# Kernel optimization log

Measured on AMD Instinct MI355X. Metric: run time of the kernel, lower is better.

The kernel has to match this reference:

```python
import jax, jax.numpy as jnp
import numpy as np

LN2 = 0.6931471805599453

def _logcosh(z):
    # numerically stable log(cosh(z)) = logaddexp(z, -z) - log(2)
    return jnp.logaddexp(z, -z) - LN2

def _logpsi(z, W, b, a):
    # RBM log-amplitude. z: [..., N] -> scalar per leading dims
    return z @ a + jnp.sum(_logcosh(z @ W + b), axis=-1)

def setup_inputs() -> dict:
    key = jax.random.key(0)
    k0, k1, k2, k3, k4 = jax.random.split(key, 5)
    B, N, H = 64, 512, 2048
    # spin configurations (sign pattern; flips y_k = x with site k negated work for any real values)
    x = jnp.sign(jax.random.normal(k0, (B, N), dtype=jnp.float32))
    # small init so exp(logpsi_y - logpsi_x) stays well-scaled
    W = 0.01 * jax.random.normal(k1, (N, H), dtype=jnp.float32)
    b = 0.01 * jax.random.normal(k2, (H,), dtype=jnp.float32)
    a = 0.01 * jax.random.normal(k3, (N,), dtype=jnp.float32)
    # per-connection operator matrix elements O(x, y_k)
    Oxy = jax.random.normal(k4, (N,), dtype=jnp.float32)
    return {"x": x, "W": W, "b": b, "a": a, "Oxy": Oxy}

def reference(x, W, b, a, Oxy):
    # eval_local_operator, vmapped over a batch of configurations.
    # operator.conn(x): y[k] = x with spin k flipped, with matrix element Oxy[k].
    B, N = x.shape
    flip = 1.0 - 2.0 * jnp.eye(N, dtype=x.dtype)          # [K=N, N]
    y = x[:, None, :] * flip[None, :, :]                  # [B, K, N] connected states
    logpsi_x = _logpsi(x, W, b, a)                        # [B]
    logpsi_y = _logpsi(y, W, b, a)                        # [B, K]
    # Oxy @ exp(logpsi_y - logpsi_x) per sample
    return jnp.einsum('k,bk->b', Oxy, jnp.exp(logpsi_y - logpsi_x[:, None]))
```

## Files before the change

### kernel.cpp

```cpp
#include <hip/hip_runtime.h>
#include <hip/hip_bf16.h>
#include <math.h>

constexpr int NB = 64;
constexpr int NN = 512;
constexpr int NH = 2048;
constexpr float LN2 = 0.6931471805599453f;

constexpr size_t OFF_TT = 0;

__global__ __launch_bounds__(512) void k_theta(const float* __restrict__ W,
                                               const float* __restrict__ x,
                                               const float* __restrict__ bvec,
                                               float* __restrict__ Tt,
                                               float* __restrict__ out) {
    __shared__ float sm[10240];
    int tid = threadIdx.x;
    int gb = blockIdx.x;
    int ht = gb & 31;
    int bt = gb >> 5;
    {
        int j = tid >> 5, c = tid & 31;
        const float4* xr = (const float4*)(x + (size_t)(bt * 16 + j) * NN);
#pragma unroll
        for (int i = 0; i < 4; i++) {
            float4 v = xr[c + i * 32];
            int n0 = (c + i * 32) * 4;
            sm[(n0 + 0) * 20 + j] = v.x;
            sm[(n0 + 1) * 20 + j] = v.y;
            sm[(n0 + 2) * 20 + j] = v.z;
            sm[(n0 + 3) * 20 + j] = v.w;
        }
    }
    __syncthreads();
    int hl = tid & 63, ns = tid >> 6;
    int h  = ht * 64 + hl;
    float acc[16];
#pragma unroll
    for (int j = 0; j < 16; j++) acc[j] = 0.f;
    const float* wp = W + h;
#pragma unroll 4
    for (int n = ns * 64; n < ns * 64 + 64; n++) {
        float w = wp[(size_t)n * NH];
        const float4* xv = (const float4*)(sm + n * 20);
        float4 a0 = xv[0], a1 = xv[1], a2 = xv[2], a3 = xv[3];
        acc[0]  = fmaf(a0.x, w, acc[0]);  acc[1]  = fmaf(a0.y, w, acc[1]);
        acc[2]  = fmaf(a0.z, w, acc[2]);  acc[3]  = fmaf(a0.w, w, acc[3]);
        acc[4]  = fmaf(a1.x, w, acc[4]);  acc[5]  = fmaf(a1.y, w, acc[5]);
        acc[6]  = fmaf(a1.z, w, acc[6]);  acc[7]  = fmaf(a1.w, w, acc[7]);
        acc[8]  = fmaf(a2.x, w, acc[8]);  acc[9]  = fmaf(a2.y, w, acc[9]);
        acc[10] = fmaf(a2.z, w, acc[10]); acc[11] = fmaf(a2.w, w, acc[11]);
        acc[12] = fmaf(a3.x, w, acc[12]); acc[13] = fmaf(a3.y, w, acc[13]);
        acc[14] = fmaf(a3.z, w, acc[14]); acc[15] = fmaf(a3.w, w, acc[15]);
    }
    __syncthreads();
    float4* r4 = (float4*)sm;
#pragma unroll
    for (int q = 0; q < 4; q++)
        r4[(ns * 1024 + hl * 16) / 4 + q] =
            make_float4(acc[q*4], acc[q*4+1], acc[q*4+2], acc[q*4+3]);
    __syncthreads();
#pragma unroll
    for (int o = tid; o < 1024; o += 512) {
        int hl2 = o >> 4, j2 = o & 15;
        float th = bvec[ht * 64 + hl2];
#pragma unroll
        for (int n2 = 0; n2 < 8; n2++) th += sm[n2 * 1024 + hl2 * 16 + j2];
        float ay = fabsf(th);
        float e  = __expf(-2.0f * ay);
        Tt[(size_t)(ht * 64 + hl2) * NB + bt * 16 + j2] =
            copysignf((1.0f - e) / (1.0f + e), th);
    }
    if (gb == 0 && tid < NB) out[tid] = 0.f;
}

__global__ __launch_bounds__(512) void k_main(const float* __restrict__ W,
                                              const float* __restrict__ Tt,
                                              const float* __restrict__ x,
                                              const float* __restrict__ a,
                                              const float* __restrict__ Oxy,
                                              float* __restrict__ out) {
    __shared__ float t2s[2 * NH];
    __shared__ float red[16 * NB];
    int tid = threadIdx.x;
    int lane = tid & 63, wv = tid >> 6;
    int k0 = __builtin_amdgcn_readfirstlane(blockIdx.x * 2);
    int hb = wv * 256;

    const float2* w0 = (const float2*)(W + (size_t)k0 * NH + hb);
    const float2* w1 = (const float2*)(W + (size_t)(k0 + 1) * NH + hb);
    float lc0 = 0.f, lc1 = 0.f;
#pragma unroll
    for (int i = 0; i < 2; i++) {
        float2 wa = w0[lane + i * 64];
        float2 wb = w1[lane + i * 64];
        float in[4] = {wa.x, wa.y, wb.x, wb.y};
        float t[4];
#pragma unroll
        for (int j = 0; j < 4; j++) {
            float y  = 2.0f * in[j];
            float ay = fabsf(y);
            float e  = __expf(-2.0f * ay);
            t[j] = copysignf((1.0f - e) / (1.0f + e), y);
            float l = ay + __logf(1.0f + e) - LN2;
            if (j < 2) lc0 += l; else lc1 += l;
        }
        int h2 = hb + (lane + i * 64) * 2;
        *(float4*)&t2s[h2 * 2] = make_float4(t[0], t[2], t[1], t[3]);
    }
#pragma unroll
    for (int off = 32; off > 0; off >>= 1) {
        lc0 += __shfl_xor(lc0, off);
        lc1 += __shfl_xor(lc1, off);
    }
    float ms0 = -x[(size_t)lane * NN + k0];
    float ms1 = -x[(size_t)lane * NN + k0 + 1];
    __syncthreads();

    float lp0 = lc0, lp1 = lc1;
    for (int h0 = hb; h0 < hb + 256; h0 += 32) {
        float p0 = 1.f, p1 = 1.f;
#pragma unroll
        for (int hh = 0; hh < 32; hh++) {
            int h = h0 + hh;
            float2 t = *(const float2*)&t2s[h * 2];
            float T = Tt[(size_t)h * NB + lane];
            p0 *= fmaf(t.x * T, ms0, 1.0f);
            p1 *= fmaf(t.y * T, ms1, 1.0f);
        }
        lp0 += __logf(p0);
        lp1 += __logf(p1);
    }
    red[(wv * 2 + 0) * NB + lane] = lp0;
    red[(wv * 2 + 1) * NB + lane] = lp1;
    __syncthreads();
    if (tid < NB) {
        float d0 = 2.0f * ms0 * a[k0];
        float d1 = 2.0f * ms1 * a[k0 + 1];
#pragma unroll
        for (int w2 = 0; w2 < 8; w2++) {
            d0 += red[(w2 * 2 + 0) * NB + tid];
            d1 += red[(w2 * 2 + 1) * NB + tid];
        }
        float c = Oxy[k0] * __expf(d0) + Oxy[k0 + 1] * __expf(d1);
        atomicAdd(&out[tid], c);
    }
}

extern "C" void kernel_launch(void* const* d_in, const int* in_sizes, int n_in,
                              void* d_out, int out_size, void* d_ws, size_t ws_size,
                              hipStream_t stream) {
    const float* x    = (const float*)d_in[0];
    const float* W    = (const float*)d_in[1];
    const float* bvec = (const float*)d_in[2];
    const float* a    = (const float*)d_in[3];
    const float* Oxy  = (const float*)d_in[4];
    float* out = (float*)d_out;

    float* Tt = (float*)d_ws + OFF_TT;

    k_theta<<<128, 512, 0, stream>>>(W, x, bvec, Tt, out);
    k_main<<<NN / 2, 512, 0, stream>>>(W, Tt, x, a, Oxy, out);
}
```

Before: 90.39 us.

## Fuse theta and main kernels into one cooperative kernel with grid sync

Merges the two kernel launches into a single cooperative launch of 256 blocks. Phase one computes the tanh(theta) table with 8-batch tiles over 256 blocks, then a grid-wide sync hands off to the per-flip product phase. The T table is also re-laid out in groups of four h values so the inner loop issues float4 loads, and the two per-site tanh vectors are split into separate shared arrays. This removes a launch gap and the separate kernel's tail at the cost of grid-sync overhead and a cooperative-launch requirement.

```diff
diff --git a/kernel.cpp b/kernel.cpp
--- a/kernel.cpp
+++ b/kernel.cpp
@@ -1,149 +1,151 @@
 #include <hip/hip_runtime.h>
-#include <hip/hip_bf16.h>
+#include <hip/hip_cooperative_groups.h>
 #include <math.h>
+
+namespace cg = cooperative_groups;
 
 constexpr int NB = 64;
 constexpr int NN = 512;
 constexpr int NH = 2048;
 constexpr float LN2 = 0.6931471805599453f;
 
-constexpr size_t OFF_TT = 0;
 
-__global__ __launch_bounds__(512) void k_theta(const float* __restrict__ W,
+__global__ __launch_bounds__(512) void k_fused(const float* __restrict__ W,
                                                const float* __restrict__ x,
                                                const float* __restrict__ bvec,
-                                               float* __restrict__ Tt,
+                                               const float* __restrict__ a,
+                                               const float* __restrict__ Oxy,
+                                               float* __restrict__ Tt4,
                                                float* __restrict__ out) {
-    __shared__ float sm[10240];
+    __shared__ float sm[6144];
     int tid = threadIdx.x;
-    int gb = blockIdx.x;
-    int ht = gb & 31;
-    int bt = gb >> 5;
+    int bid = blockIdx.x;
+
     {
-        int j = tid >> 5, c = tid & 31;
-        const float4* xr = (const float4*)(x + (size_t)(bt * 16 + j) * NN);
+        int ht  = bid & 31;
+        int btb = bid >> 5;
+        {
+            int j = tid >> 6, c = tid & 63;
+            const float4* xr = (const float4*)(x + (size_t)(btb * 8 + j) * NN);
 #pragma unroll
-        for (int i = 0; i < 4; i++) {
-            float4 v = xr[c + i * 32];
-            int n0 = (c + i * 32) * 4;
-            sm[(n0 + 0) * 20 + j] = v.x;
-            sm[(n0 + 1) * 20 + j] = v.y;
-            sm[(n0 + 2) * 20 + j] = v.z;
-            sm[(n0 + 3) * 20 + j] = v.w;
+            for (int i = 0; i < 2; i++) {
+                float4 v = xr[c + i * 64];
+                int n0 = (c + i * 64) * 4;
+                sm[(n0 + 0) * 12 + j] = v.x;
+                sm[(n0 + 1) * 12 + j] = v.y;
+                sm[(n0 + 2) * 12 + j] = v.z;
+                sm[(n0 + 3) * 12 + j] = v.w;
+            }
         }
-    }
-    __syncthreads();
-    int hl = tid & 63, ns = tid >> 6;
-    int h  = ht * 64 + hl;
-    float acc[16];
+        __syncthreads();
+        int hl = tid & 63, ns = tid >> 6;
+        float acc[8];
 #pragma unroll
-    for (int j = 0; j < 16; j++) acc[j] = 0.f;
-    const float* wp = W + h;
+        for (int q = 0; q < 8; q++) acc[q] = 0.f;
+        const float* wp = W + ht * 64 + hl;
 #pragma unroll 4
-    for (int n = ns * 64; n < ns * 64 + 64; n++) {
-        float w = wp[(size_t)n * NH];
-        const float4* xv = (const float4*)(sm + n * 20);
-        float4 a0 = xv[0], a1 = xv[1], a2 = xv[2], a3 = xv[3];
-        acc[0]  = fmaf(a0.x, w, acc[0]);  acc[1]  = fmaf(a0.y, w, acc[1]);
-        acc[2]  = fmaf(a0.z, w, acc[2]);  acc[3]  = fmaf(a0.w, w, acc[3]);
-        acc[4]  = fmaf(a1.x, w, acc[4]);  acc[5]  = fmaf(a1.y, w, acc[5]);
-        acc[6]  = fmaf(a1.z, w, acc[6]);  acc[7]  = fmaf(a1.w, w, acc[7]);
-        acc[8]  = fmaf(a2.x, w, acc[8]);  acc[9]  = fmaf(a2.y, w, acc[9]);
-        acc[10] = fmaf(a2.z, w, acc[10]); acc[11] = fmaf(a2.w, w, acc[11]);
-        acc[12] = fmaf(a3.x, w, acc[12]); acc[13] = fmaf(a3.y, w, acc[13]);
-        acc[14] = fmaf(a3.z, w, acc[14]); acc[15] = fmaf(a3.w, w, acc[15]);
-    }
-    __syncthreads();
-    float4* r4 = (float4*)sm;
-#pragma unroll
-    for (int q = 0; q < 4; q++)
-        r4[(ns * 1024 + hl * 16) / 4 + q] =
-            make_float4(acc[q*4], acc[q*4+1], acc[q*4+2], acc[q*4+3]);
-    __syncthreads();
-#pragma unroll
-    for (int o = tid; o < 1024; o += 512) {
-        int hl2 = o >> 4, j2 = o & 15;
+        for (int n = ns * 64; n < ns * 64 + 64; n++) {
+            float w = wp[(size_t)n * NH];
+            const float4* xv = (const float4*)(sm + n * 12);
+            float4 a0 = xv[0], a1 = xv[1];
+            acc[0] = fmaf(a0.x, w, acc[0]); acc[1] = fmaf(a0.y, w, acc[1]);
+            acc[2] = fmaf(a0.z, w, acc[2]); acc[3] = fmaf(a0.w, w, acc[3]);
+            acc[4] = fmaf(a1.x, w, acc[4]); acc[5] = fmaf(a1.y, w, acc[5]);
+            acc[6] = fmaf(a1.z, w, acc[6]); acc[7] = fmaf(a1.w, w, acc[7]);
+        }
+        __syncthreads();
+        float4* r4 = (float4*)sm;
+        r4[ns * 128 + hl * 2 + 0] = make_float4(acc[0], acc[1], acc[2], acc[3]);
+        r4[ns * 128 + hl * 2 + 1] = make_float4(acc[4], acc[5], acc[6], acc[7]);
+        __syncthreads();
+        int hl2 = tid >> 3, j2 = tid & 7;
         float th = bvec[ht * 64 + hl2];
 #pragma unroll
-        for (int n2 = 0; n2 < 8; n2++) th += sm[n2 * 1024 + hl2 * 16 + j2];
+        for (int n2 = 0; n2 < 8; n2++) th += sm[n2 * 512 + hl2 * 8 + j2];
         float ay = fabsf(th);
         float e  = __expf(-2.0f * ay);
-        Tt[(size_t)(ht * 64 + hl2) * NB + bt * 16 + j2] =
-            copysignf((1.0f - e) / (1.0f + e), th);
+        float T  = copysignf((1.0f - e) / (1.0f + e), th);
+        int h = ht * 64 + hl2, b = btb * 8 + j2;
+        Tt4[(size_t)(h >> 2) * 256 + b * 4 + (h & 3)] = T;
+        if (bid == 0 && tid < NB) out[tid] = 0.f;
     }
-    if (gb == 0 && tid < NB) out[tid] = 0.f;
-}
+    cg::this_grid().sync();
 
-__global__ __launch_bounds__(512) void k_main(const float* __restrict__ W,
-                                              const float* __restrict__ Tt,
-                                              const float* __restrict__ x,
-                                              const float* __restrict__ a,
-                                              const float* __restrict__ Oxy,
-                                              float* __restrict__ out) {
-    __shared__ float t2s[2 * NH];
-    __shared__ float red[16 * NB];
-    int tid = threadIdx.x;
-    int lane = tid & 63, wv = tid >> 6;
-    int k0 = __builtin_amdgcn_readfirstlane(blockIdx.x * 2);
-    int hb = wv * 256;
+    {
+        float* t2s0 = sm;
+        float* t2s1 = sm + NH;
+        float* red  = sm + 2 * NH;
+        int lane = tid & 63, wv = tid >> 6;
+        int k0 = __builtin_amdgcn_readfirstlane(blockIdx.x * 2);
+        int hb = wv * 256;
 
-    const float2* w0 = (const float2*)(W + (size_t)k0 * NH + hb);
-    const float2* w1 = (const float2*)(W + (size_t)(k0 + 1) * NH + hb);
-    float lc0 = 0.f, lc1 = 0.f;
+        const float2* w0 = (const float2*)(W + (size_t)k0 * NH + hb);
+        const float2* w1 = (const float2*)(W + (size_t)(k0 + 1) * NH + hb);
+        float lc0 = 0.f, lc1 = 0.f;
 #pragma unroll
-    for (int i = 0; i < 2; i++) {
-        float2 wa = w0[lane + i * 64];
-        float2 wb = w1[lane + i * 64];
-        float in[4] = {wa.x, wa.y, wb.x, wb.y};
-        float t[4];
+        for (int i = 0; i < 2; i++) {
+            float2 wa = w0[lane + i * 64];
+            float2 wb = w1[lane + i * 64];
+            float in[4] = {wa.x, wa.y, wb.x, wb.y};
+            float t[4];
 #pragma unroll
-        for (int j = 0; j < 4; j++) {
-            float y  = 2.0f * in[j];
-            float ay = fabsf(y);
-            float e  = __expf(-2.0f * ay);
-            t[j] = copysignf((1.0f - e) / (1.0f + e), y);
-            float l = ay + __logf(1.0f + e) - LN2;
-            if (j < 2) lc0 += l; else lc1 += l;
+            for (int q = 0; q < 4; q++) {
+                float y  = 2.0f * in[q];
+                float ay = fabsf(y);
+                float e  = __expf(-2.0f * ay);
+                t[q] = copysignf((1.0f - e) / (1.0f + e), y);
+                float l = ay + __logf(1.0f + e) - LN2;
+                if (q < 2) lc0 += l; else lc1 += l;
+            }
+            int h2 = hb + (lane + i * 64) * 2;
+            *(float2*)&t2s0[h2] = make_float2(t[0], t[1]);
+            *(float2*)&t2s1[h2] = make_float2(t[2], t[3]);
         }
-        int h2 = hb + (lane + i * 64) * 2;
-        *(float4*)&t2s[h2 * 2] = make_float4(t[0], t[2], t[1], t[3]);
-    }
 #pragma unroll
-    for (int off = 32; off > 0; off >>= 1) {
-        lc0 += __shfl_xor(lc0, off);
-        lc1 += __shfl_xor(lc1, off);
-    }
-    float ms0 = -x[(size_t)lane * NN + k0];
-    float ms1 = -x[(size_t)lane * NN + k0 + 1];
-    __syncthreads();
+        for (int off = 32; off > 0; off >>= 1) {
+            lc0 += __shfl_xor(lc0, off);
+            lc1 += __shfl_xor(lc1, off);
+        }
+        float ms0 = -x[(size_t)lane * NN + k0];
+        float ms1 = -x[(size_t)lane * NN + k0 + 1];
+        __syncthreads();
 
-    float lp0 = lc0, lp1 = lc1;
-    for (int h0 = hb; h0 < hb + 256; h0 += 32) {
-        float p0 = 1.f, p1 = 1.f;
+        float lp0 = lc0, lp1 = lc1;
+        const float* tp = Tt4 + lane * 4;
+        for (int h0 = hb; h0 < hb + 256; h0 += 32) {
+            float p0 = 1.f, p1 = 1.f;
 #pragma unroll
-        for (int hh = 0; hh < 32; hh++) {
-            int h = h0 + hh;
-            float2 t = *(const float2*)&t2s[h * 2];
-            float T = Tt[(size_t)h * NB + lane];
-            p0 *= fmaf(t.x * T, ms0, 1.0f);
-            p1 *= fmaf(t.y * T, ms1, 1.0f);
+            for (int hh = 0; hh < 32; hh += 4) {
+                int h = h0 + hh;
+                float4 T  = *(const float4*)(tp + (size_t)h * 64);
+                float4 t0 = *(const float4*)&t2s0[h];
+                float4 t1 = *(const float4*)&t2s1[h];
+                p0 *= fmaf(t0.x * T.x, ms0, 1.f);
+                p0 *= fmaf(t0.y * T.y, ms0, 1.f);
+                p0 *= fmaf(t0.z * T.z, ms0, 1.f);
+                p0 *= fmaf(t0.w * T.w, ms0, 1.f);
+                p1 *= fmaf(t1.x * T.x, ms1, 1.f);
+                p1 *= fmaf(t1.y * T.y, ms1, 1.f);
+                p1 *= fmaf(t1.z * T.z, ms1, 1.f);
+                p1 *= fmaf(t1.w * T.w, ms1, 1.f);
+            }
+            lp0 += __logf(p0);
+            lp1 += __logf(p1);
         }
-        lp0 += __logf(p0);
-        lp1 += __logf(p1);
-    }
-    red[(wv * 2 + 0) * NB + lane] = lp0;
-    red[(wv * 2 + 1) * NB + lane] = lp1;
-    __syncthreads();
-    if (tid < NB) {
-        float d0 = 2.0f * ms0 * a[k0];
-        float d1 = 2.0f * ms1 * a[k0 + 1];
+        red[(wv * 2 + 0) * NB + lane] = lp0;
+        red[(wv * 2 + 1) * NB + lane] = lp1;
+        __syncthreads();
+        if (tid < NB) {
+            float d0 = 2.0f * ms0 * a[k0];
+            float d1 = 2.0f * ms1 * a[k0 + 1];
 #pragma unroll
-        for (int w2 = 0; w2 < 8; w2++) {
-            d0 += red[(w2 * 2 + 0) * NB + tid];
-            d1 += red[(w2 * 2 + 1) * NB + tid];
+            for (int w2 = 0; w2 < 8; w2++) {
+                d0 += red[(w2 * 2 + 0) * NB + tid];
+                d1 += red[(w2 * 2 + 1) * NB + tid];
+            }
+            float c = Oxy[k0] * __expf(d0) + Oxy[k0 + 1] * __expf(d1);
+            atomicAdd(&out[tid], c);
         }
-        float c = Oxy[k0] * __expf(d0) + Oxy[k0 + 1] * __expf(d1);
-        atomicAdd(&out[tid], c);
     }
 }
 
@@ -156,9 +158,9 @@
     const float* a    = (const float*)d_in[3];
     const float* Oxy  = (const float*)d_in[4];
     float* out = (float*)d_out;
+    float* Tt4 = (float*)d_ws;
 
-    float* Tt = (float*)d_ws + OFF_TT;
-
-    k_theta<<<128, 512, 0, stream>>>(W, x, bvec, Tt, out);
-    k_main<<<NN / 2, 512, 0, stream>>>(W, Tt, x, a, Oxy, out);
+    void* args[] = {(void*)&W, (void*)&x, (void*)&bvec, (void*)&a, (void*)&Oxy,
+                    (void*)&Tt4, (void*)&out};
+    hipLaunchCooperativeKernel((void*)k_fused, dim3(256), dim3(512), args, 0, stream);
 }
```

Result: slower. 125.7 us (+39.1%).
